# Performance work log

Hardware: AMD Instinct MI355X
Metric: run time of the kernel (lower is better)

## Reference

```python
import jax, jax.numpy as jnp
import numpy as np

B, N, D = 8, 4096, 768  # batch, node_size, mem_dim (== in_dim, num_layers=1)


def setup_inputs() -> dict:
    key = jax.random.key(0)
    k1, k2, k3, k4 = jax.random.split(key, 4)
    scale = 0.02
    return {
        "nodes": jax.random.normal(k1, (B, N, D), dtype=jnp.float32),
        "adj": jax.random.uniform(k2, (B, N, N), dtype=jnp.float32),
        "W0": jax.random.normal(k3, (D, D), dtype=jnp.float32) * scale,
        "b0": jnp.zeros((D,), dtype=jnp.float32),
        "Wout": jax.random.normal(k4, (D, D), dtype=jnp.float32) * scale,
        "bout": jnp.zeros((D,), dtype=jnp.float32),
    }


def reference(nodes, adj, W0, b0, Wout, bout):
    # DSGCN forward (num_layers=1, dropout=identity/eval mode).
    # torch Linear: y = x @ W.T + b, W shape [out, in].
    denom = jnp.sum(adj, axis=2, keepdims=True) + 1.0          # [B, N, 1] row-degree + 1
    xW = jnp.einsum("bnd,hd->bnh", nodes, W0) + b0              # bxW == W0(gcn_inputs) since outputs==inputs at l=0
    AxW = jnp.einsum("bnm,bmh->bnh", adj, xW)                   # batched SpMM (dense here)
    gAxWs = jax.nn.relu((AxW + xW) / denom)                     # fused add/div/relu
    gcn_outputs = gAxWs + nodes                                 # residual with gcn_inputs
    out = jnp.einsum("bnh,oh->bno", gcn_outputs, Wout) + bout   # linear_output
    return out
```

## Files before the change

kernel.cpp:

```cpp
#include <hip/hip_runtime.h>
#include <hip/hip_bf16.h>
#include <hip/hip_fp8.h>

using bf16 = __hip_bfloat16;
typedef __attribute__((ext_vector_type(8))) short bf16x8;
typedef __attribute__((ext_vector_type(4))) float f32x4;
typedef __attribute__((ext_vector_type(4))) int i32x4;
typedef __attribute__((ext_vector_type(8))) int i32x8;

#define B_DIM 8
#define N_DIM 4096
#define D_DIM 768
#define BN_DIM 32768

__device__ __forceinline__ void gload_lds16(const void* g, void* l) {
  __builtin_amdgcn_global_load_lds(
      (const __attribute__((address_space(1))) void*)g,
      (__attribute__((address_space(3))) void*)l, 16, 0, 0);
}

__device__ __forceinline__ unsigned char to_fp8(float v) {
  return __hip_fp8_e4m3(v).__x;
}

__global__ __launch_bounds__(256) void prep_adj_k(const float* __restrict__ adj,
                                                  unsigned char* __restrict__ adj_f4,
                                                  float* __restrict__ rdenom) {
  const int row = blockIdx.x;
  const int n = row & (N_DIM - 1);
  const int t = threadIdx.x;
  const float* __restrict__ ar = adj + (size_t)row * N_DIM;
  unsigned char* __restrict__ orow = adj_f4 + (size_t)row * (N_DIM / 2);
  float s = 0.f;
#pragma unroll
  for (int j = 0; j < N_DIM; j += 1024) {
    const int c = j + t * 4;
    float4 v = *reinterpret_cast<const float4*>(ar + c);
    s += v.x + v.y + v.z + v.w;
    if (n >= c && n < c + 4) (&v.x)[n - c] += 1.0f;
    const unsigned n0 = (unsigned)(v.x * 2.f + 0.5f);
    const unsigned n1 = (unsigned)(v.y * 2.f + 0.5f);
    const unsigned n2 = (unsigned)(v.z * 2.f + 0.5f);
    const unsigned n3 = (unsigned)(v.w * 2.f + 0.5f);
    *reinterpret_cast<unsigned short*>(orow + (c >> 1)) =
        (unsigned short)(n0 | (n1 << 4) | (n2 << 8) | (n3 << 12));
  }
#pragma unroll
  for (int off = 32; off > 0; off >>= 1) s += __shfl_down(s, off);
  __shared__ float red[4];
  const int lane = t & 63, wv = t >> 6;
  if (lane == 0) red[wv] = s;
  __syncthreads();
  if (t == 0) rdenom[row] = 1.0f / (red[0] + red[1] + red[2] + red[3] + 1.0f);
}

__global__ __launch_bounds__(256) void cvt_bf16_k(const float* __restrict__ in,
                                                  bf16* __restrict__ out, int n4) {
  const int i = blockIdx.x * 256 + threadIdx.x;
  if (i >= n4) return;
  float4 v = reinterpret_cast<const float4*>(in)[i];
  union { bf16 h[4]; uint2 u; } pk;
  pk.h[0] = __float2bfloat16(v.x);
  pk.h[1] = __float2bfloat16(v.y);
  pk.h[2] = __float2bfloat16(v.z);
  pk.h[3] = __float2bfloat16(v.w);
  reinterpret_cast<uint2*>(out)[i] = pk.u;
}

__global__ __launch_bounds__(256) void cvt_fp8_k(const float* __restrict__ in,
                                                 unsigned char* __restrict__ out, int n4) {
  const int i = blockIdx.x * 256 + threadIdx.x;
  if (i >= n4) return;
  float4 v = reinterpret_cast<const float4*>(in)[i];
  union { unsigned char b[4]; unsigned int u; } pk;
  pk.b[0] = to_fp8(v.x);
  pk.b[1] = to_fp8(v.y);
  pk.b[2] = to_fp8(v.z);
  pk.b[3] = to_fp8(v.w);
  reinterpret_cast<unsigned int*>(out)[i] = pk.u;
}

__global__ __launch_bounds__(256) void gemm1_f8_k(
    const unsigned char* __restrict__ A, const unsigned char* __restrict__ Bt,
    int NT, size_t lda, size_t ldb, int gx, int gy,
    const float* __restrict__ e_bias, unsigned char* __restrict__ xwt) {
  __shared__ unsigned char lds[2][32768];
  const int nwg = gridDim.x;
  const int q8 = nwg >> 3;
  const int bid = blockIdx.x;
  const int wg = (bid & 7) * q8 + (bid >> 3);
  const int bx = wg % gx;
  const int by = (wg / gx) % gy;

  const int tid = threadIdx.x;
  const int lane = tid & 63, wave = tid >> 6;
  const int wr = wave >> 1, wc = wave & 1;
  const int row0 = by * 128, col0 = bx * 128;
  const unsigned char* __restrict__ Ab = A + (size_t)row0 * lda;
  const unsigned char* __restrict__ Bb = Bt + (size_t)col0 * ldb;

  f32x4 acc[4][4];
#pragma unroll
  for (int i = 0; i < 4; ++i)
#pragma unroll
    for (int j = 0; j < 4; ++j) acc[i][j] = 0.f;

  const int l15 = lane & 15, l7 = lane & 7;
  const int kc = (lane >> 4) * 2;
  const int o0 = l15 * 128 + ((kc ^ l7) << 4);
  const int o1 = l15 * 128 + (((kc + 1) ^ l7) << 4);

#pragma unroll
  for (int it = 0; it < 4; ++it) {
    const int q = it * 256 + tid;
    const int r = q >> 3;
    const int gc = (q & 7) ^ (r & 7);
    const int lb16 = (it * 256 + wave * 64) * 16;
    gload_lds16(Ab + (size_t)r * lda + gc * 16, &lds[0][0] + lb16);
    gload_lds16(Bb + (size_t)r * ldb + gc * 16, &lds[0][16384] + lb16);
  }

  for (int t = 0; t < NT; ++t) {
    const int cur = t & 1;
    if (t != NT - 1) {
      const int kt = (t + 1) << 7;
      unsigned char* la = &lds[cur ^ 1][0];
      unsigned char* lb = &lds[cur ^ 1][16384];
#pragma unroll
      for (int it = 0; it < 4; ++it) {
        const int q = it * 256 + tid;
        const int r = q >> 3;
        const int gc = (q & 7) ^ (r & 7);
        const int lb16 = (it * 256 + wave * 64) * 16;
        gload_lds16(Ab + (size_t)r * lda + kt + gc * 16, la + lb16);
        gload_lds16(Bb + (size_t)r * ldb + kt + gc * 16, lb + lb16);
      }
      asm volatile("s_waitcnt vmcnt(8)" ::: "memory");
    } else {
      asm volatile("s_waitcnt vmcnt(0)" ::: "memory");
    }
    __builtin_amdgcn_s_barrier();
    __builtin_amdgcn_sched_barrier(0);
    const unsigned char* la = &lds[cur][0];
    const unsigned char* lb = &lds[cur][16384];
    union frag { i32x4 q[2]; i32x8 o; };
    frag bfr[4];
#pragma unroll
    for (int ni = 0; ni < 4; ++ni) {
      const unsigned char* p = lb + (wc * 64 + ni * 16) * 128;
      bfr[ni].q[0] = *reinterpret_cast<const i32x4*>(p + o0);
      bfr[ni].q[1] = *reinterpret_cast<const i32x4*>(p + o1);
    }
#pragma unroll
    for (int mi = 0; mi < 4; ++mi) {
      frag afr;
      const unsigned char* p = la + (wr * 64 + mi * 16) * 128;
      afr.q[0] = *reinterpret_cast<const i32x4*>(p + o0);
      afr.q[1] = *reinterpret_cast<const i32x4*>(p + o1);
#pragma unroll
      for (int ni = 0; ni < 4; ++ni)
        acc[mi][ni] = __builtin_amdgcn_mfma_scale_f32_16x16x128_f8f6f4(
            afr.o, bfr[ni].o, acc[mi][ni], 0, 0,
            0, 0x7F7F7F7F, 0, 0x7F7F7F7F);
    }
    __builtin_amdgcn_sched_barrier(0);
    __builtin_amdgcn_s_barrier();
  }

  const int erow = wr * 64 + (lane >> 4) * 4;
  const int ecol = wc * 64 + (lane & 15);
#pragma unroll
  for (int mi = 0; mi < 4; ++mi) {
#pragma unroll
    for (int i = 0; i < 4; ++i) {
      const int h = row0 + erow + mi * 16 + i;
      const float bias = e_bias[h];
      unsigned char* __restrict__ xrow = xwt + (size_t)h * BN_DIM;
#pragma unroll
      for (int ni = 0; ni < 4; ++ni) {
        const int cn = col0 + ecol + ni * 16;
        xrow[cn] = to_fp8(acc[mi][ni][i] + bias);
      }
    }
  }
}

__global__ __launch_bounds__(256, 3) void gemm2_f4_k(
    const unsigned char* __restrict__ A4,
    const unsigned char* __restrict__ B8,
    const float* __restrict__ rdenom, const float* __restrict__ nodes,
    bf16* __restrict__ gout_all) {
  __shared__ unsigned char lds[2][24576];
  const int nwg = gridDim.x;
  const int q8n = nwg >> 3;
  const int bid = blockIdx.x;
  const int wg = (bid & 7) * q8n + (bid >> 3);
  const int gx = D_DIM / 128;
  const int gy = N_DIM / 128;
  const int bx = wg % gx;
  const int tmp = wg / gx;
  const int by = tmp % gy;
  const int z = tmp / gy;

  const int tid = threadIdx.x;
  const int lane = tid & 63, wave = tid >> 6;
  const int wr = wave >> 1, wc = wave & 1;
  const int row0 = by * 128, col0 = bx * 128;
  const unsigned char* __restrict__ Ab = A4 + ((size_t)z * N_DIM + row0) * (N_DIM / 2);
  const unsigned char* __restrict__ Bb = B8 + (size_t)col0 * BN_DIM + (size_t)z * N_DIM;

  f32x4 acc[4][4];
#pragma unroll
  for (int i = 0; i < 4; ++i)
#pragma unroll
    for (int j = 0; j < 4; ++j) acc[i][j] = 0.f;

  const int l15 = lane & 15, l7 = lane & 7;
  const int kc = (lane >> 4) * 2;
  const int o0 = l15 * 128 + ((kc ^ l7) << 4);
  const int o1 = l15 * 128 + (((kc + 1) ^ l7) << 4);
  const int ac = lane >> 4;

#define STAGE2(buf, kt)                                                          \
  {                                                                              \
    const int kA = (kt) << 6;                  \
    const int kB = (kt) << 7;                                                    \
    _Pragma("unroll") for (int it = 0; it < 2; ++it) {                           \
      const int q = it * 256 + tid;                                              \
      const int r = q >> 2, p = q & 3;                                           \
      const int lc = (p + 4 - ((r >> 1) & 3)) & 3;                               \
      gload_lds16(Ab + (size_t)r * (N_DIM / 2) + kA + lc * 16,                   \
                  &lds[buf][0] + (it * 256 + wave * 64) * 16);                   \
    }                                                                            \
    _Pragma("unroll") for (int it = 0; it < 4; ++it) {                           \
      const int q = it * 256 + tid;                                              \
      const int r = q >> 3;                                                      \
      const int gc = (q & 7) ^ (r & 7);                                          \
      gload_lds16(Bb + (size_t)r * BN_DIM + kB + gc * 16,                        \
                  &lds[buf][8192] + (it * 256 + wave * 64) * 16);                \
    }                                                                            \
  }

  STAGE2(0, 0);

  for (int t = 0; t < 32; ++t) {
    const int cur = t & 1;
    if (t != 31) {
      STAGE2(cur ^ 1, t + 1);
      asm volatile("s_waitcnt vmcnt(6)" ::: "memory");
    } else {
      asm volatile("s_waitcnt vmcnt(0)" ::: "memory");
    }
    __builtin_amdgcn_s_barrier();
    __builtin_amdgcn_sched_barrier(0);
    const unsigned char* la = &lds[cur][0];
    const unsigned char* lb = &lds[cur][8192];
    union frag { i32x4 q[2]; i32x8 o; };
    frag bfr[4];
#pragma unroll
    for (int ni = 0; ni < 4; ++ni) {
      const unsigned char* p = lb + (wc * 64 + ni * 16) * 128;
      bfr[ni].q[0] = *reinterpret_cast<const i32x4*>(p + o0);
      bfr[ni].q[1] = *reinterpret_cast<const i32x4*>(p + o1);
    }
#pragma unroll
    for (int mi = 0; mi < 4; ++mi) {
      const int ar = wr * 64 + mi * 16 + l15;
      const int p = (ac + (ar >> 1)) & 3;
      frag afr;
      afr.q[0] = *reinterpret_cast<const i32x4*>(la + ar * 64 + (p << 4));
      afr.q[1] = i32x4{0, 0, 0, 0};
#pragma unroll
      for (int ni = 0; ni < 4; ++ni)
        acc[mi][ni] = __builtin_amdgcn_mfma_scale_f32_16x16x128_f8f6f4(
            afr.o, bfr[ni].o, acc[mi][ni], 4, 0,
            0, 0x7F7F7F7F, 0, 0x7F7F7F7F);
    }
    __builtin_amdgcn_sched_barrier(0);
    __builtin_amdgcn_s_barrier();
  }
#undef STAGE2

  const int erow = wr * 64 + (lane >> 4) * 4;
  const int ecol = wc * 64 + (lane & 15);
  bf16* __restrict__ gout = gout_all + (size_t)z * N_DIM * D_DIM;
  const float* __restrict__ nb = nodes + (size_t)z * N_DIM * D_DIM;
  const float* __restrict__ rdz = rdenom + z * N_DIM;
#pragma unroll
  for (int mi = 0; mi < 4; ++mi) {
#pragma unroll
    for (int i = 0; i < 4; ++i) {
      const int gm = row0 + erow + mi * 16 + i;
      const float rd = rdz[gm];
      const float* __restrict__ nrow = nb + (size_t)gm * D_DIM;
      bf16* __restrict__ grow = gout + (size_t)gm * D_DIM;
#pragma unroll
      for (int ni = 0; ni < 4; ++ni) {
        const int h = col0 + ecol + ni * 16;
        const float v = fmaxf(acc[mi][ni][i] * rd, 0.f) + nrow[h];
        grow[h] = __float2bfloat16(v);
      }
    }
  }
}

__global__ __launch_bounds__(256) void gemm3_k(
    const bf16* __restrict__ A,
    const bf16* __restrict__ Bt,
    const float* __restrict__ bias, float* __restrict__ out) {
  __shared__ bf16 lds[2][2][128 * 32];
  const int nwg = gridDim.x;
  const int q8 = nwg >> 3;
  const int bid = blockIdx.x;
  const int wg = (bid & 7) * q8 + (bid >> 3);
  const int gx = D_DIM / 128;
  const int bx = wg % gx;
  const int by = wg / gx;

  const int tid = threadIdx.x;
  const int lane = tid & 63, wave = tid >> 6;
  const int wr = wave >> 1, wc = wave & 1;
  const int row0 = by * 128, col0 = bx * 128;
  const bf16* __restrict__ Ab = A + (size_t)row0 * D_DIM;
  const bf16* __restrict__ Bb = Bt + (size_t)col0 * D_DIM;

  f32x4 acc[4][4];
#pragma unroll
  for (int i = 0; i < 4; ++i)
#pragma unroll
    for (int j = 0; j < 4; ++j) acc[i][j] = 0.f;

  const int rowA = wr * 64 + (lane & 15);
  const int rowB = wc * 64 + (lane & 15);
  const int kc = lane >> 4;

#pragma unroll
  for (int j = 0; j < 2; ++j) {
    const int c = j * 256 + tid;
    const int r = c >> 2;
    const int gc = (c & 3) ^ (r & 3);
    const size_t go = (size_t)r * D_DIM + gc * 8;
    const int lbase = (j * 256 + wave * 64) * 8;
    gload_lds16(Ab + go, &lds[0][0][0] + lbase);
    gload_lds16(Bb + go, &lds[0][1][0] + lbase);
  }

  for (int t = 0; t < 24; ++t) {
    const int cur = t & 1;
    if (t != 23) {
      const int kt = (t + 1) * 32;
      bf16* la = &lds[cur ^ 1][0][0];
      bf16* lb = &lds[cur ^ 1][1][0];
#pragma unroll
      for (int j = 0; j < 2; ++j) {
        const int c = j * 256 + tid;
        const int r = c >> 2;
        const int gc = (c & 3) ^ (r & 3);
        const size_t go = (size_t)r * D_DIM + kt + gc * 8;
        const int lbase = (j * 256 + wave * 64) * 8;
        gload_lds16(Ab + go, la + lbase);
        gload_lds16(Bb + go, lb + lbase);
      }
      asm volatile("s_waitcnt vmcnt(4)" ::: "memory");
    } else {
      asm volatile("s_waitcnt vmcnt(0)" ::: "memory");
    }
    __builtin_amdgcn_s_barrier();
    __builtin_amdgcn_sched_barrier(0);
    const bf16* la = &lds[cur][0][0];
    const bf16* lb = &lds[cur][1][0];
    bf16x8 af[4], bv[4];
#pragma unroll
    for (int mi = 0; mi < 4; ++mi) {
      const int rr = rowA + mi * 16;
      af[mi] = *reinterpret_cast<const bf16x8*>(&la[rr * 32 + ((kc ^ (rr & 3)) << 3)]);
    }
#pragma unroll
    for (int ni = 0; ni < 4; ++ni) {
      const int rr = rowB + ni * 16;
      bv[ni] = *reinterpret_cast<const bf16x8*>(&lb[rr * 32 + ((kc ^ (rr & 3)) << 3)]);
    }
#pragma unroll
    for (int mi = 0; mi < 4; ++mi)
#pragma unroll
      for (int ni = 0; ni < 4; ++ni)
        acc[mi][ni] = __builtin_amdgcn_mfma_f32_16x16x32_bf16(af[mi], bv[ni],
                                                              acc[mi][ni], 0, 0, 0);
    __builtin_amdgcn_sched_barrier(0);
    __builtin_amdgcn_s_barrier();
  }

  const int erow = wr * 64 + (lane >> 4) * 4;
  const int ecol = wc * 64 + (lane & 15);
#pragma unroll
  for (int mi = 0; mi < 4; ++mi) {
#pragma unroll
    for (int i = 0; i < 4; ++i) {
      const int gm = row0 + erow + mi * 16 + i;
#pragma unroll
      for (int ni = 0; ni < 4; ++ni) {
        const int h = col0 + ecol + ni * 16;
        out[(size_t)gm * D_DIM + h] = acc[mi][ni][i] + bias[h];
      }
    }
  }
}

extern "C" void kernel_launch(void* const* d_in, const int* in_sizes, int n_in,
                              void* d_out, int out_size, void* d_ws, size_t ws_size,
                              hipStream_t stream) {
  const float* nodes = (const float*)d_in[0];
  const float* adj   = (const float*)d_in[1];
  const float* W0    = (const float*)d_in[2];
  const float* b0    = (const float*)d_in[3];
  const float* Wout  = (const float*)d_in[4];
  const float* bout  = (const float*)d_in[5];
  float* out = (float*)d_out;

  char* ws = (char*)d_ws;
  size_t off = 0;
  auto alloc = [&](size_t bytes) {
    void* p = ws + off;
    off += (bytes + 255) & ~(size_t)255;
    return p;
  };
  const size_t ND = (size_t)B_DIM * N_DIM;
  unsigned char* adj_f4   = (unsigned char*)alloc((size_t)B_DIM * N_DIM * N_DIM / 2);
  unsigned char* nodes_f8 = (unsigned char*)alloc(ND * D_DIM);
  unsigned char* xwt      = (unsigned char*)alloc((size_t)D_DIM * BN_DIM);
  bf16* gbf       = (bf16*)alloc(ND * D_DIM * 2);
  unsigned char* w0_f8 = (unsigned char*)alloc((size_t)D_DIM * D_DIM);
  bf16* wout_bf   = (bf16*)alloc((size_t)D_DIM * D_DIM * 2);
  float* rdenom   = (float*)alloc(ND * 4);

  prep_adj_k<<<dim3(32768), dim3(256), 0, stream>>>(adj, adj_f4, rdenom);
  {
    const int n4 = (int)(ND * D_DIM / 4);
    cvt_fp8_k<<<dim3((n4 + 255) / 256), dim3(256), 0, stream>>>(nodes, nodes_f8, n4);
    const int w4 = D_DIM * D_DIM / 4;
    cvt_fp8_k<<<dim3((w4 + 255) / 256), dim3(256), 0, stream>>>(W0, w0_f8, w4);
    cvt_bf16_k<<<dim3((w4 + 255) / 256), dim3(256), 0, stream>>>(Wout, wout_bf, w4);
  }

  gemm1_f8_k<<<dim3((BN_DIM / 128) * (D_DIM / 128)), dim3(256), 0, stream>>>(
      w0_f8, nodes_f8, 6, D_DIM, D_DIM,
      BN_DIM / 128, D_DIM / 128, b0, xwt);

  gemm2_f4_k<<<dim3((D_DIM / 128) * (N_DIM / 128) * B_DIM), dim3(256), 0, stream>>>(
      adj_f4, xwt, rdenom, nodes, gbf);

  gemm3_k<<<dim3((D_DIM / 128) * (BN_DIM / 128)), dim3(256), 0, stream>>>(
      gbf, wout_bf, bout, out);
}
```

Before: 347.9 us.

## Enlarge gemm2 tile to 256 rows with 8 waves and interleaved staged pipeline

The adjacency GEMM now uses 512-thread workgroups, each covering a 256x128 output tile, with a larger LDS double buffer. The main loop is split into four phases that interleave global-to-LDS loads of A and B, LDS fragment reads and MFMA groups under barriers and s_setprio. The goal is to reuse each B tile across more rows and to hide load latency behind MFMA work. The extra barriers per iteration and the larger LDS footprint lower occupancy and add synchronization cost.

New measurement: 353.8 us. Within noise of the previous version (+1.7%).

```diff
diff --git a/kernel.cpp b/kernel.cpp
--- a/kernel.cpp
+++ b/kernel.cpp
@@ -185,18 +185,18 @@
   }
 }
 
-__global__ __launch_bounds__(256, 3) void gemm2_f4_k(
+__global__ __launch_bounds__(512) void gemm2_f4_k(
     const unsigned char* __restrict__ A4,
     const unsigned char* __restrict__ B8,
     const float* __restrict__ rdenom, const float* __restrict__ nodes,
     bf16* __restrict__ gout_all) {
-  __shared__ unsigned char lds[2][24576];
+  __shared__ unsigned char lds[2][32768];
   const int nwg = gridDim.x;
   const int q8n = nwg >> 3;
   const int bid = blockIdx.x;
   const int wg = (bid & 7) * q8n + (bid >> 3);
   const int gx = D_DIM / 128;
-  const int gy = N_DIM / 128;
+  const int gy = N_DIM / 256;
   const int bx = wg % gx;
   const int tmp = wg / gx;
   const int by = tmp % gy;
@@ -205,7 +205,7 @@
   const int tid = threadIdx.x;
   const int lane = tid & 63, wave = tid >> 6;
   const int wr = wave >> 1, wc = wave & 1;
-  const int row0 = by * 128, col0 = bx * 128;
+  const int row0 = by * 256, col0 = bx * 128;
   const unsigned char* __restrict__ Ab = A4 + ((size_t)z * N_DIM + row0) * (N_DIM / 2);
   const unsigned char* __restrict__ Bb = B8 + (size_t)col0 * BN_DIM + (size_t)z * N_DIM;
 
@@ -221,65 +221,104 @@
   const int o1 = l15 * 128 + (((kc + 1) ^ l7) << 4);
   const int ac = lane >> 4;
 
-#define STAGE2(buf, kt)                                                          \
+#define STAGE_A(buf, kt_)                                                        \
   {                                                                              \
-    const int kA = (kt) << 6;                  \
-    const int kB = (kt) << 7;                                                    \
+    const int kA = (kt_) << 6;                                                   \
     _Pragma("unroll") for (int it = 0; it < 2; ++it) {                           \
-      const int q = it * 256 + tid;                                              \
+      const int q = it * 512 + tid;                                              \
       const int r = q >> 2, p = q & 3;                                           \
       const int lc = (p + 4 - ((r >> 1) & 3)) & 3;                               \
       gload_lds16(Ab + (size_t)r * (N_DIM / 2) + kA + lc * 16,                   \
-                  &lds[buf][0] + (it * 256 + wave * 64) * 16);                   \
+                  &lds[buf][0] + (it * 512 + wave * 64) * 16);                   \
     }                                                                            \
-    _Pragma("unroll") for (int it = 0; it < 4; ++it) {                           \
-      const int q = it * 256 + tid;                                              \
+  }
+#define STAGE_B(buf, kt_)                                                        \
+  {                                                                              \
+    const int kB = (kt_) << 7;                                                   \
+    _Pragma("unroll") for (int it = 0; it < 2; ++it) {                           \
+      const int q = it * 512 + tid;                                              \
       const int r = q >> 3;                                                      \
       const int gc = (q & 7) ^ (r & 7);                                          \
       gload_lds16(Bb + (size_t)r * BN_DIM + kB + gc * 16,                        \
-                  &lds[buf][8192] + (it * 256 + wave * 64) * 16);                \
+                  &lds[buf][16384] + (it * 512 + wave * 64) * 16);               \
     }                                                                            \
   }
 
-  STAGE2(0, 0);
+  STAGE_A(0, 0);
+  STAGE_B(0, 0);
+  asm volatile("s_waitcnt vmcnt(0)" ::: "memory");
+  __builtin_amdgcn_s_barrier();
+
+  union frag { i32x4 q[2]; i32x8 o; };
+  const i32x4 z4 = {0, 0, 0, 0};
 
   for (int t = 0; t < 32; ++t) {
-    const int cur = t & 1;
-    if (t != 31) {
-      STAGE2(cur ^ 1, t + 1);
-      asm volatile("s_waitcnt vmcnt(6)" ::: "memory");
-    } else {
-      asm volatile("s_waitcnt vmcnt(0)" ::: "memory");
-    }
-    __builtin_amdgcn_s_barrier();
-    __builtin_amdgcn_sched_barrier(0);
+    const int cur = t & 1, nxt = cur ^ 1;
     const unsigned char* la = &lds[cur][0];
-    const unsigned char* lb = &lds[cur][8192];
-    union frag { i32x4 q[2]; i32x8 o; };
-    frag bfr[4];
-#pragma unroll
-    for (int ni = 0; ni < 4; ++ni) {
-      const unsigned char* p = lb + (wc * 64 + ni * 16) * 128;
-      bfr[ni].q[0] = *reinterpret_cast<const i32x4*>(p + o0);
-      bfr[ni].q[1] = *reinterpret_cast<const i32x4*>(p + o1);
-    }
-#pragma unroll
-    for (int mi = 0; mi < 4; ++mi) {
-      const int ar = wr * 64 + mi * 16 + l15;
-      const int p = (ac + (ar >> 1)) & 3;
-      frag afr;
-      afr.q[0] = *reinterpret_cast<const i32x4*>(la + ar * 64 + (p << 4));
-      afr.q[1] = i32x4{0, 0, 0, 0};
-#pragma unroll
-      for (int ni = 0; ni < 4; ++ni)
-        acc[mi][ni] = __builtin_amdgcn_mfma_scale_f32_16x16x128_f8f6f4(
-            afr.o, bfr[ni].o, acc[mi][ni], 4, 0,
-            0, 0x7F7F7F7F, 0, 0x7F7F7F7F);
-    }
-    __builtin_amdgcn_sched_barrier(0);
-    __builtin_amdgcn_s_barrier();
-  }
-#undef STAGE2
+    const unsigned char* lb = &lds[cur][16384];
+    frag a0, a1, a2, a3, b0, b1, b2, b3;
+
+#define RD_A(dst, mi_)                                                           \
+    {                                                                            \
+      const int ar = wr * 64 + (mi_)*16 + l15;                                   \
+      const int p = (ac + (ar >> 1)) & 3;                                        \
+      dst.q[0] = *reinterpret_cast<const i32x4*>(la + ar * 64 + (p << 4));       \
+      dst.q[1] = z4;                                                             \
+    }
+#define RD_B(dst, ni_)                                                           \
+    {                                                                            \
+      const unsigned char* p = lb + (wc * 64 + (ni_)*16) * 128;                  \
+      dst.q[0] = *reinterpret_cast<const i32x4*>(p + o0);                        \
+      dst.q[1] = *reinterpret_cast<const i32x4*>(p + o1);                        \
+    }
+#define MFMA4(m0_, m1_, n0_, n1_, am0, am1, bn0, bn1)                            \
+    __builtin_amdgcn_s_setprio(1);                                               \
+    acc[m0_][n0_] = __builtin_amdgcn_mfma_scale_f32_16x16x128_f8f6f4(            \
+        am0.o, bn0.o, acc[m0_][n0_], 4, 0, 0, 0x7F7F7F7F, 0, 0x7F7F7F7F);        \
+    acc[m0_][n1_] = __builtin_amdgcn_mfma_scale_f32_16x16x128_f8f6f4(            \
+        am0.o, bn1.o, acc[m0_][n1_], 4, 0, 0, 0x7F7F7F7F, 0, 0x7F7F7F7F);        \
+    acc[m1_][n0_] = __builtin_amdgcn_mfma_scale_f32_16x16x128_f8f6f4(            \
+        am1.o, bn0.o, acc[m1_][n0_], 4, 0, 0, 0x7F7F7F7F, 0, 0x7F7F7F7F);        \
+    acc[m1_][n1_] = __builtin_amdgcn_mfma_scale_f32_16x16x128_f8f6f4(            \
+        am1.o, bn1.o, acc[m1_][n1_], 4, 0, 0, 0x7F7F7F7F, 0, 0x7F7F7F7F);        \
+    __builtin_amdgcn_s_setprio(0);
+
+    if (t != 31) STAGE_A(nxt, t + 1);
+    RD_A(a0, 0) RD_A(a1, 1) RD_B(b0, 0) RD_B(b1, 1)
+    __builtin_amdgcn_sched_barrier(0);
+    __builtin_amdgcn_s_barrier();
+    asm volatile("s_waitcnt lgkmcnt(0)" ::: "memory");
+    __builtin_amdgcn_sched_barrier(0);
+    MFMA4(0, 1, 0, 1, a0, a1, b0, b1)
+    __builtin_amdgcn_s_barrier();
+
+    if (t != 31) STAGE_B(nxt, t + 1);
+    RD_A(a2, 2) RD_A(a3, 3)
+    __builtin_amdgcn_sched_barrier(0);
+    __builtin_amdgcn_s_barrier();
+    asm volatile("s_waitcnt lgkmcnt(0)" ::: "memory");
+    __builtin_amdgcn_sched_barrier(0);
+    MFMA4(2, 3, 0, 1, a2, a3, b0, b1)
+    __builtin_amdgcn_s_barrier();
+
+    RD_B(b2, 2) RD_B(b3, 3)
+    __builtin_amdgcn_sched_barrier(0);
+    __builtin_amdgcn_s_barrier();
+    asm volatile("s_waitcnt lgkmcnt(0)" ::: "memory");
+    __builtin_amdgcn_sched_barrier(0);
+    MFMA4(0, 1, 2, 3, a0, a1, b2, b3)
+    __builtin_amdgcn_s_barrier();
+
+    asm volatile("s_waitcnt vmcnt(0)" ::: "memory");
+    __builtin_amdgcn_s_barrier();
+    MFMA4(2, 3, 2, 3, a2, a3, b2, b3)
+    __builtin_amdgcn_s_barrier();
+#undef RD_A
+#undef RD_B
+#undef MFMA4
+  }
+#undef STAGE_A
+#undef STAGE_B
 
   const int erow = wr * 64 + (lane >> 4) * 4;
   const int ecol = wc * 64 + (lane & 15);
@@ -446,7 +485,7 @@
       w0_f8, nodes_f8, 6, D_DIM, D_DIM,
       BN_DIM / 128, D_DIM / 128, b0, xwt);
 
-  gemm2_f4_k<<<dim3((D_DIM / 128) * (N_DIM / 128) * B_DIM), dim3(256), 0, stream>>>(
+  gemm2_f4_k<<<dim3((D_DIM / 128) * (N_DIM / 256) * B_DIM), dim3(512), 0, stream>>>(
       adj_f4, xwt, rdenom, nodes, gbf);
 
   gemm3_k<<<dim3((D_DIM / 128) * (BN_DIM / 128)), dim3(256), 0, stream>>>(
```

## Fuse prep kernels and switch aggregation GEMM to 32x32 MFMA with smaller K tiles

Applied to the files above, without the earlier changes.

Merges the adjacency prep and the three dtype conversion kernels into one launch, which saves launch overhead and lets them run concurrently. Rewrites the aggregation GEMM to use 32x32x64 scaled MFMA instructions with a K step of 64, halving LDS per block and raising the occupancy hint from 3 to 6. The per-iteration loads and barriers double in count (64 steps instead of 32), and the swizzle patterns are redone for the new layout. The epilogue is adapted to the 32x32 accumulator register layout.

New measurement: 1.336 ms. 3.84x slower.

```diff
diff --git a/kernel.cpp b/kernel.cpp
--- a/kernel.cpp
+++ b/kernel.cpp
@@ -5,6 +5,7 @@
 using bf16 = __hip_bfloat16;
 typedef __attribute__((ext_vector_type(8))) short bf16x8;
 typedef __attribute__((ext_vector_type(4))) float f32x4;
+typedef __attribute__((ext_vector_type(16))) float f32x16;
 typedef __attribute__((ext_vector_type(4))) int i32x4;
 typedef __attribute__((ext_vector_type(8))) int i32x8;
 
@@ -23,61 +24,64 @@
   return __hip_fp8_e4m3(v).__x;
 }
 
-__global__ __launch_bounds__(256) void prep_adj_k(const float* __restrict__ adj,
-                                                  unsigned char* __restrict__ adj_f4,
-                                                  float* __restrict__ rdenom) {
-  const int row = blockIdx.x;
-  const int n = row & (N_DIM - 1);
+__global__ __launch_bounds__(256) void prep_all_k(
+    const float* __restrict__ adj, unsigned char* __restrict__ adj_f4,
+    float* __restrict__ rdenom,
+    const float* __restrict__ nodes, unsigned char* __restrict__ nodes_f8,
+    const float* __restrict__ W0, unsigned char* __restrict__ w0_f8,
+    const float* __restrict__ Wout, bf16* __restrict__ wout_bf) {
+  const int blk = blockIdx.x;
   const int t = threadIdx.x;
-  const float* __restrict__ ar = adj + (size_t)row * N_DIM;
-  unsigned char* __restrict__ orow = adj_f4 + (size_t)row * (N_DIM / 2);
-  float s = 0.f;
-#pragma unroll
-  for (int j = 0; j < N_DIM; j += 1024) {
-    const int c = j + t * 4;
-    float4 v = *reinterpret_cast<const float4*>(ar + c);
-    s += v.x + v.y + v.z + v.w;
-    if (n >= c && n < c + 4) (&v.x)[n - c] += 1.0f;
-    const unsigned n0 = (unsigned)(v.x * 2.f + 0.5f);
-    const unsigned n1 = (unsigned)(v.y * 2.f + 0.5f);
-    const unsigned n2 = (unsigned)(v.z * 2.f + 0.5f);
-    const unsigned n3 = (unsigned)(v.w * 2.f + 0.5f);
-    *reinterpret_cast<unsigned short*>(orow + (c >> 1)) =
-        (unsigned short)(n0 | (n1 << 4) | (n2 << 8) | (n3 << 12));
-  }
-#pragma unroll
-  for (int off = 32; off > 0; off >>= 1) s += __shfl_down(s, off);
-  __shared__ float red[4];
-  const int lane = t & 63, wv = t >> 6;
-  if (lane == 0) red[wv] = s;
-  __syncthreads();
-  if (t == 0) rdenom[row] = 1.0f / (red[0] + red[1] + red[2] + red[3] + 1.0f);
-}
-
-__global__ __launch_bounds__(256) void cvt_bf16_k(const float* __restrict__ in,
-                                                  bf16* __restrict__ out, int n4) {
-  const int i = blockIdx.x * 256 + threadIdx.x;
-  if (i >= n4) return;
-  float4 v = reinterpret_cast<const float4*>(in)[i];
-  union { bf16 h[4]; uint2 u; } pk;
-  pk.h[0] = __float2bfloat16(v.x);
-  pk.h[1] = __float2bfloat16(v.y);
-  pk.h[2] = __float2bfloat16(v.z);
-  pk.h[3] = __float2bfloat16(v.w);
-  reinterpret_cast<uint2*>(out)[i] = pk.u;
-}
-
-__global__ __launch_bounds__(256) void cvt_fp8_k(const float* __restrict__ in,
-                                                 unsigned char* __restrict__ out, int n4) {
-  const int i = blockIdx.x * 256 + threadIdx.x;
-  if (i >= n4) return;
-  float4 v = reinterpret_cast<const float4*>(in)[i];
-  union { unsigned char b[4]; unsigned int u; } pk;
-  pk.b[0] = to_fp8(v.x);
-  pk.b[1] = to_fp8(v.y);
-  pk.b[2] = to_fp8(v.z);
-  pk.b[3] = to_fp8(v.w);
-  reinterpret_cast<unsigned int*>(out)[i] = pk.u;
+  if (blk < 32768) {
+    const int row = blk;
+    const int n = row & (N_DIM - 1);
+    const float* __restrict__ ar = adj + (size_t)row * N_DIM;
+    unsigned char* __restrict__ orow = adj_f4 + (size_t)row * (N_DIM / 2);
+    float s = 0.f;
+#pragma unroll
+    for (int j = 0; j < N_DIM; j += 1024) {
+      const int c = j + t * 4;
+      float4 v = *reinterpret_cast<const float4*>(ar + c);
+      s += v.x + v.y + v.z + v.w;
+      if (n >= c && n < c + 4) (&v.x)[n - c] += 1.0f;
+      const unsigned n0 = (unsigned)(v.x * 2.f + 0.5f);
+      const unsigned n1 = (unsigned)(v.y * 2.f + 0.5f);
+      const unsigned n2 = (unsigned)(v.z * 2.f + 0.5f);
+      const unsigned n3 = (unsigned)(v.w * 2.f + 0.5f);
+      *reinterpret_cast<unsigned short*>(orow + (c >> 1)) =
+          (unsigned short)(n0 | (n1 << 4) | (n2 << 8) | (n3 << 12));
+    }
+#pragma unroll
+    for (int off = 32; off > 0; off >>= 1) s += __shfl_down(s, off);
+    __shared__ float red[4];
+    const int lane = t & 63, wv = t >> 6;
+    if (lane == 0) red[wv] = s;
+    __syncthreads();
+    if (t == 0) rdenom[row] = 1.0f / (red[0] + red[1] + red[2] + red[3] + 1.0f);
+    return;
+  }
+  const int j = (blk - 32768) * 256 + t;
+  if (j < 6291456) {
+    float4 v = reinterpret_cast<const float4*>(nodes)[j];
+    union { unsigned char b[4]; unsigned int u; } pk;
+    pk.b[0] = to_fp8(v.x); pk.b[1] = to_fp8(v.y);
+    pk.b[2] = to_fp8(v.z); pk.b[3] = to_fp8(v.w);
+    reinterpret_cast<unsigned int*>(nodes_f8)[j] = pk.u;
+  } else if (j < 6291456 + 147456) {
+    const int k = j - 6291456;
+    float4 v = reinterpret_cast<const float4*>(W0)[k];
+    union { unsigned char b[4]; unsigned int u; } pk;
+    pk.b[0] = to_fp8(v.x); pk.b[1] = to_fp8(v.y);
+    pk.b[2] = to_fp8(v.z); pk.b[3] = to_fp8(v.w);
+    reinterpret_cast<unsigned int*>(w0_f8)[k] = pk.u;
+  } else {
+    const int k = j - 6291456 - 147456;
+    float4 v = reinterpret_cast<const float4*>(Wout)[k];
+    union { bf16 h[4]; uint2 u; } pk;
+    pk.h[0] = __float2bfloat16(v.x); pk.h[1] = __float2bfloat16(v.y);
+    pk.h[2] = __float2bfloat16(v.z); pk.h[3] = __float2bfloat16(v.w);
+    reinterpret_cast<uint2*>(wout_bf)[k] = pk.u;
+  }
 }
 
 __global__ __launch_bounds__(256) void gemm1_f8_k(
@@ -185,12 +189,12 @@
   }
 }
 
-__global__ __launch_bounds__(256, 3) void gemm2_f4_k(
+__global__ __launch_bounds__(256, 6) void gemm2_f4_k(
     const unsigned char* __restrict__ A4,
     const unsigned char* __restrict__ B8,
     const float* __restrict__ rdenom, const float* __restrict__ nodes,
     bf16* __restrict__ gout_all) {
-  __shared__ unsigned char lds[2][24576];
+  __shared__ unsigned char lds[2][12288];
   const int nwg = gridDim.x;
   const int q8n = nwg >> 3;
   const int bid = blockIdx.x;
@@ -209,96 +213,95 @@
   const unsigned char* __restrict__ Ab = A4 + ((size_t)z * N_DIM + row0) * (N_DIM / 2);
   const unsigned char* __restrict__ Bb = B8 + (size_t)col0 * BN_DIM + (size_t)z * N_DIM;
 
-  f32x4 acc[4][4];
-#pragma unroll
-  for (int i = 0; i < 4; ++i)
-#pragma unroll
-    for (int j = 0; j < 4; ++j) acc[i][j] = 0.f;
-
-  const int l15 = lane & 15, l7 = lane & 7;
-  const int kc = (lane >> 4) * 2;
-  const int o0 = l15 * 128 + ((kc ^ l7) << 4);
-  const int o1 = l15 * 128 + (((kc + 1) ^ l7) << 4);
-  const int ac = lane >> 4;
-
-#define STAGE2(buf, kt)                                                          \
+  f32x16 acc[2][2];
+#pragma unroll
+  for (int i = 0; i < 2; ++i)
+#pragma unroll
+    for (int j = 0; j < 2; ++j) acc[i][j] = 0.f;
+
+  const int l31 = lane & 31;
+  const int h = lane >> 5;
+
+#define STAGE(buf, kt_)                                                          \
   {                                                                              \
-    const int kA = (kt) << 6;                  \
-    const int kB = (kt) << 7;                                                    \
+    const int kA = (kt_) << 5;                  \
+    const int kB = (kt_) << 6;                                    \
+    {                                                                            \
+      const int r = tid >> 1, p = tid & 1;                                       \
+      const int sp = p ^ ((r >> 2) & 1);                                         \
+      gload_lds16(Ab + (size_t)r * (N_DIM / 2) + kA + sp * 16,                   \
+                  &lds[buf][0] + (wave * 64) * 16);                              \
+    }                                                                            \
     _Pragma("unroll") for (int it = 0; it < 2; ++it) {                           \
       const int q = it * 256 + tid;                                              \
       const int r = q >> 2, p = q & 3;                                           \
-      const int lc = (p + 4 - ((r >> 1) & 3)) & 3;                               \
-      gload_lds16(Ab + (size_t)r * (N_DIM / 2) + kA + lc * 16,                   \
-                  &lds[buf][0] + (it * 256 + wave * 64) * 16);                   \
+      const int sp = p ^ ((r & 3) ^ ((r >> 2) & 3));                             \
+      gload_lds16(Bb + (size_t)r * BN_DIM + kB + sp * 16,                        \
+                  &lds[buf][4096] + (it * 256 + wave * 64) * 16);                \
     }                                                                            \
-    _Pragma("unroll") for (int it = 0; it < 4; ++it) {                           \
-      const int q = it * 256 + tid;                                              \
-      const int r = q >> 3;                                                      \
-      const int gc = (q & 7) ^ (r & 7);                                          \
-      gload_lds16(Bb + (size_t)r * BN_DIM + kB + gc * 16,                        \
-                  &lds[buf][8192] + (it * 256 + wave * 64) * 16);                \
-    }                                                                            \
-  }
-
-  STAGE2(0, 0);
-
-  for (int t = 0; t < 32; ++t) {
+  }
+
+  STAGE(0, 0);
+
+  union frag { i32x4 q[2]; i32x8 o; };
+  const i32x4 z4 = {0, 0, 0, 0};
+
+  for (int t = 0; t < 64; ++t) {
     const int cur = t & 1;
-    if (t != 31) {
-      STAGE2(cur ^ 1, t + 1);
-      asm volatile("s_waitcnt vmcnt(6)" ::: "memory");
+    if (t != 63) {
+      STAGE(cur ^ 1, t + 1);
+      asm volatile("s_waitcnt vmcnt(3)" ::: "memory");
     } else {
       asm volatile("s_waitcnt vmcnt(0)" ::: "memory");
     }
     __builtin_amdgcn_s_barrier();
     __builtin_amdgcn_sched_barrier(0);
     const unsigned char* la = &lds[cur][0];
-    const unsigned char* lb = &lds[cur][8192];
-    union frag { i32x4 q[2]; i32x8 o; };
-    frag bfr[4];
-#pragma unroll
-    for (int ni = 0; ni < 4; ++ni) {
-      const unsigned char* p = lb + (wc * 64 + ni * 16) * 128;
-      bfr[ni].q[0] = *reinterpret_cast<const i32x4*>(p + o0);
-      bfr[ni].q[1] = *reinterpret_cast<const i32x4*>(p + o1);
-    }
-#pragma unroll
-    for (int mi = 0; mi < 4; ++mi) {
-      const int ar = wr * 64 + mi * 16 + l15;
-      const int p = (ac + (ar >> 1)) & 3;
-      frag afr;
-      afr.q[0] = *reinterpret_cast<const i32x4*>(la + ar * 64 + (p << 4));
-      afr.q[1] = i32x4{0, 0, 0, 0};
-#pragma unroll
-      for (int ni = 0; ni < 4; ++ni)
-        acc[mi][ni] = __builtin_amdgcn_mfma_scale_f32_16x16x128_f8f6f4(
-            afr.o, bfr[ni].o, acc[mi][ni], 4, 0,
+    const unsigned char* lb = &lds[cur][4096];
+    frag afr[2], bfr[2];
+#pragma unroll
+    for (int mi = 0; mi < 2; ++mi) {
+      const int ra = wr * 64 + mi * 32 + l31;
+      afr[mi].q[0] = *reinterpret_cast<const i32x4*>(
+          la + ra * 32 + ((h ^ ((ra >> 2) & 1)) << 4));
+      afr[mi].q[1] = z4;
+    }
+#pragma unroll
+    for (int ni = 0; ni < 2; ++ni) {
+      const int rb = wc * 64 + ni * 32 + l31;
+      const int sB = (rb & 3) ^ ((rb >> 2) & 3);
+      const int g0 = (2 * h) ^ sB;
+      bfr[ni].q[0] = *reinterpret_cast<const i32x4*>(lb + rb * 64 + g0 * 16);
+      bfr[ni].q[1] = *reinterpret_cast<const i32x4*>(lb + rb * 64 + (g0 ^ 1) * 16);
+    }
+#pragma unroll
+    for (int mi = 0; mi < 2; ++mi)
+#pragma unroll
+      for (int ni = 0; ni < 2; ++ni)
+        acc[mi][ni] = __builtin_amdgcn_mfma_scale_f32_32x32x64_f8f6f4(
+            afr[mi].o, bfr[ni].o, acc[mi][ni], 4, 0,
             0, 0x7F7F7F7F, 0, 0x7F7F7F7F);
-    }
-    __builtin_amdgcn_sched_barrier(0);
-    __builtin_amdgcn_s_barrier();
-  }
-#undef STAGE2
-
-  const int erow = wr * 64 + (lane >> 4) * 4;
-  const int ecol = wc * 64 + (lane & 15);
+    __builtin_amdgcn_sched_barrier(0);
+    __builtin_amdgcn_s_barrier();
+  }
+#undef STAGE
+
   bf16* __restrict__ gout = gout_all + (size_t)z * N_DIM * D_DIM;
   const float* __restrict__ nb = nodes + (size_t)z * N_DIM * D_DIM;
   const float* __restrict__ rdz = rdenom + z * N_DIM;
 #pragma unroll
-  for (int mi = 0; mi < 4; ++mi) {
-#pragma unroll
-    for (int i = 0; i < 4; ++i) {
-      const int gm = row0 + erow + mi * 16 + i;
+  for (int mi = 0; mi < 2; ++mi) {
+#pragma unroll
+    for (int reg = 0; reg < 16; ++reg) {
+      const int gm = row0 + wr * 64 + mi * 32 + 4 * h + 8 * (reg >> 2) + (reg & 3);
       const float rd = rdz[gm];
       const float* __restrict__ nrow = nb + (size_t)gm * D_DIM;
       bf16* __restrict__ grow = gout + (size_t)gm * D_DIM;
 #pragma unroll
-      for (int ni = 0; ni < 4; ++ni) {
-        const int h = col0 + ecol + ni * 16;
-        const float v = fmaxf(acc[mi][ni][i] * rd, 0.f) + nrow[h];
-        grow[h] = __float2bfloat16(v);
+      for (int ni = 0; ni < 2; ++ni) {
+        const int col = col0 + wc * 64 + ni * 32 + l31;
+        const float v = fmaxf(acc[mi][ni][reg] * rd, 0.f) + nrow[col];
+        grow[col] = __float2bfloat16(v);
       }
     }
   }
@@ -433,14 +436,8 @@
   bf16* wout_bf   = (bf16*)alloc((size_t)D_DIM * D_DIM * 2);
   float* rdenom   = (float*)alloc(ND * 4);
 
-  prep_adj_k<<<dim3(32768), dim3(256), 0, stream>>>(adj, adj_f4, rdenom);
-  {
-    const int n4 = (int)(ND * D_DIM / 4);
-    cvt_fp8_k<<<dim3((n4 + 255) / 256), dim3(256), 0, stream>>>(nodes, nodes_f8, n4);
-    const int w4 = D_DIM * D_DIM / 4;
-    cvt_fp8_k<<<dim3((w4 + 255) / 256), dim3(256), 0, stream>>>(W0, w0_f8, w4);
-    cvt_bf16_k<<<dim3((w4 + 255) / 256), dim3(256), 0, stream>>>(Wout, wout_bf, w4);
-  }
+  prep_all_k<<<dim3(32768 + 25728), dim3(256), 0, stream>>>(
+      adj, adj_f4, rdenom, nodes, nodes_f8, W0, w0_f8, Wout, wout_bf);
 
   gemm1_f8_k<<<dim3((BN_DIM / 128) * (D_DIM / 128)), dim3(256), 0, stream>>>(
       w0_f8, nodes_f8, 6, D_DIM, D_DIM,
```
